# Kernel tuning notes

Measured on AMD Instinct MI355X. Metric: run time of the kernel, lower is better.

Reference implementation:

```python
import jax, jax.numpy as jnp
import numpy as np


def _chamfer_min_sqdist(a, b):
    # a: [N,3], b: [M,3] -> for each point in a, min squared distance to b. [N]
    # ||a||^2 + ||b||^2 - 2 a.b^T ; clamp tiny negatives from cancellation.
    a2 = jnp.sum(a * a, axis=-1)            # [N]
    b2 = jnp.sum(b * b, axis=-1)            # [M]
    cross = a @ b.T                          # [N,M] GEMM, K=3
    d = a2[:, None] + b2[None, :] - 2.0 * cross
    return jnp.maximum(jnp.min(d, axis=1), 0.0)


def setup_inputs() -> dict:
    key = jax.random.key(0)
    k1, k2 = jax.random.split(key)
    N = 16384
    state_x = jax.random.normal(k1, (N, 3), dtype=jnp.float32)
    target = jax.random.normal(k2, (N, 3), dtype=jnp.float32)
    return {"state_x": state_x, "target": target}


def reference(state_x, target):
    # dist1: target -> nearest in state_x ; dist2: state_x -> nearest in target
    dist1 = _chamfer_min_sqdist(target, state_x)   # [N]
    dist2 = _chamfer_min_sqdist(state_x, target)   # [N]
    loss = (jnp.mean(jnp.sqrt(dist1)) + jnp.mean(jnp.sqrt(dist2))) * 0.5
    return loss * 10.0
```

## Files before the change

kernel.cpp:

```cpp
#include <hip/hip_runtime.h>
#include <math.h>


typedef __attribute__((ext_vector_type(8)))  short bf16x8;
typedef __attribute__((ext_vector_type(16))) float f32x16;

#define S_SLICES 4

__device__ __forceinline__ unsigned enc_f32(float f) {
    int b = __float_as_int(f);
    return (b >= 0) ? ((unsigned)b | 0x80000000u) : ~(unsigned)b;
}
__device__ __forceinline__ float dec_f32(unsigned k) {
    int b = (k & 0x80000000u) ? (int)(k & 0x7FFFFFFFu) : ~(int)k;
    return __int_as_float(b);
}

__device__ __forceinline__ unsigned short f2bf(float v) {
    unsigned u = __float_as_uint(v);
    u += 0x7FFFu + ((u >> 16) & 1u);
    return (unsigned short)(u >> 16);
}
__device__ __forceinline__ float bf2f(unsigned short b) {
    unsigned u = ((unsigned)b) << 16;
    return __uint_as_float(u);
}
__device__ __forceinline__ unsigned pk2(unsigned short lo, unsigned short hi) {
    return (unsigned)lo | ((unsigned)hi << 16);
}

__device__ __forceinline__ f32x16 mfma_v(bf16x8 a, bf16x8 b, f32x16 c) {
    f32x16 d;
    asm("v_mfma_f32_32x32x16_bf16 %0, %1, %2, %3"
        : "=&v"(d) : "v"(a), "v"(b), "v"(c));
    return d;
}

__global__ __launch_bounds__(256) void chamfer_prep(
    const float* __restrict__ state_x, const float* __restrict__ target,
    uint4* __restrict__ AfragS, uint4* __restrict__ AfragT,
    uint4* __restrict__ BfragS, uint4* __restrict__ BfragT,
    unsigned* __restrict__ mins_u, float* __restrict__ out, int N)
{
    const int p = blockIdx.x * 256 + threadIdx.x;
    const float* src = (p < N) ? state_x : target;
    const int i = (p < N) ? p : p - N;

    const float x = src[3*i+0], y = src[3*i+1], z = src[3*i+2];
    const float n2 = fmaf(x, x, fmaf(y, y, z * z));

    const unsigned short hx = f2bf(x), hy = f2bf(y), hz = f2bf(z);
    const unsigned short lx = f2bf(x - bf2f(hx));
    const unsigned short ly = f2bf(y - bf2f(hy));
    const unsigned short lz = f2bf(z - bf2f(hz));
    const unsigned short mhx = f2bf(-2.0f*x), mhy = f2bf(-2.0f*y), mhz = f2bf(-2.0f*z);
    const unsigned short mlx = f2bf(-2.0f*x - bf2f(mhx));
    const unsigned short mly = f2bf(-2.0f*y - bf2f(mhy));
    const unsigned short mlz = f2bf(-2.0f*z - bf2f(mhz));
    const unsigned short hn = f2bf(n2);
    const unsigned short ln = f2bf(n2 - bf2f(hn));
    const unsigned short ONE = 0x3F80;

    uint4 A0 = make_uint4(pk2(mhx,mhy), pk2(mhz,mlx), pk2(mly,mlz), pk2(mhx,mhy));
    uint4 A1 = make_uint4(pk2(mhz,mlx), pk2(mly,mlz), pk2(hn,ln),   pk2(ONE,ONE));
    uint4 B0 = make_uint4(pk2(hx,hy), pk2(hz,hx), pk2(hy,hz), pk2(lx,ly));
    uint4 B1 = make_uint4(pk2(lz,lx), pk2(ly,lz), pk2(ONE,ONE), pk2(hn,ln));

    uint4* Aarr = (p < N) ? AfragS : AfragT;
    uint4* Barr = (p < N) ? BfragS : BfragT;
    Aarr[2*i+0] = A0;  Aarr[2*i+1] = A1;

    const int bbase = (i >> 6) * 128 + ((i >> 5) & 1) * 64 + (i & 31);
    Barr[bbase +  0] = B0;
    Barr[bbase + 32] = B1;

    mins_u[p] = 0xFFFFFFFFu;
    if (p == 0) *out = 0.0f;
}

__global__ __launch_bounds__(256, 4) void chamfer_main(
    const bf16x8* __restrict__ AfragS, const bf16x8* __restrict__ AfragT,
    const bf16x8* __restrict__ BfragS, const bf16x8* __restrict__ BfragT,
    unsigned* __restrict__ mins_u, int N, int S)
{
    const int tid  = threadIdx.x;
    const int lane = tid & 63;
    const int l31  = lane & 31;
    const int half = lane >> 5;
    const int w    = tid >> 6;

    const int bs = blockIdx.x / S;
    const int s  = blockIdx.x % S;
    const int qblk = bs * 128;

    const bf16x8* afr;
    const bf16x8* bfr;
    if (qblk < N) { afr = AfragT + (size_t)qblk * 2;       bfr = BfragS; }
    else          { afr = AfragS + (size_t)(qblk - N) * 2; bfr = BfragT; }

    const int CS = N / S;
    const int NCHUNK = CS / 1024;

    __shared__ uint4 ldsB[2048];
    const bf16x8* lb = (const bf16x8*)ldsB;

    const bf16x8 av = afr[(w * 32 + l31) * 2 + half];

    const int boff = half * 32 + l31;

    f32x16 racc, zc;
    #pragma unroll
    for (int i = 0; i < 16; ++i) { racc[i] = 3.0e38f; zc[i] = 0.0f; }

    for (int chunk = 0; chunk < NCHUNK; ++chunk) {
        {
            const uint4* src = (const uint4*)bfr
                             + ((size_t)s * CS + (size_t)chunk * 1024) * 2;
            #pragma unroll
            for (int j = 0; j < 8; ++j)
                ldsB[tid + j * 256] = src[tid + j * 256];
        }
        __syncthreads();

        #pragma unroll 1
        for (int it = 0; it < 16; ++it) {
            const bf16x8 b0 = lb[it * 128 + boff];
            const bf16x8 b1 = lb[it * 128 + 64 + boff];
            f32x16 a0 = mfma_v(av, b0, zc);
            f32x16 a1 = mfma_v(av, b1, zc);
            __builtin_amdgcn_sched_barrier(0);
            asm volatile("s_nop 7");
            asm volatile("s_nop 7");
            asm volatile("s_nop 7");
            __builtin_amdgcn_sched_barrier(0);
            #pragma unroll
            for (int i = 0; i < 16; ++i)
                racc[i] = fminf(fminf(racc[i], a0[i]), a1[i]);
        }
        __syncthreads();
    }

    float* lf = (float*)ldsB;
    const int cg = l31 >> 2, cl = l31 & 3;
    #pragma unroll
    for (int i = 0; i < 16; ++i) {
        const int row = (i & 3) + 8 * (i >> 2) + 4 * half;
        lf[w * 1024 + row * 32 + ((cg ^ (row & 7)) << 2) + cl] = racc[i];
    }
    __syncthreads();
    if (tid < 128) {
        const int r = tid & 31, wr = tid >> 5;
        const float4* rowp = (const float4*)(lf + wr * 1024 + r * 32);
        float m0 = 3.0e38f, m1 = 3.0e38f;
        #pragma unroll
        for (int g = 0; g < 8; g += 2) {
            const float4 v0 = rowp[g ^ (r & 7)];
            const float4 v1 = rowp[(g + 1) ^ (r & 7)];
            m0 = fminf(fminf(m0, v0.x), fminf(v0.y, v0.z));
            m0 = fminf(m0, v0.w);
            m1 = fminf(fminf(m1, v1.x), fminf(v1.y, v1.z));
            m1 = fminf(m1, v1.w);
        }
        atomicMin(&mins_u[qblk + wr * 32 + r], enc_f32(fminf(m0, m1)));
    }
}

__global__ __launch_bounds__(256) void chamfer_finish(
    const unsigned* __restrict__ mins_u, float* __restrict__ out, int N)
{
    const int tid = threadIdx.x;
    const int qi = blockIdx.x * 256 + tid;

    float v = sqrtf(fmaxf(dec_f32(mins_u[qi]), 0.0f));

    for (int off = 32; off > 0; off >>= 1) v += __shfl_down(v, off, 64);
    __shared__ float wsum[4];
    if ((tid & 63) == 0) wsum[tid >> 6] = v;
    __syncthreads();
    if (tid == 0) {
        const float bsum = wsum[0] + wsum[1] + wsum[2] + wsum[3];
        atomicAdd(out, bsum * 5.0f / (float)N);
    }
}

extern "C" void kernel_launch(void* const* d_in, const int* in_sizes, int n_in,
                              void* d_out, int out_size, void* d_ws, size_t ws_size,
                              hipStream_t stream)
{
    const float* state_x = (const float*)d_in[0];
    const float* target  = (const float*)d_in[1];
    float* out = (float*)d_out;

    const int N = in_sizes[0] / 3;
    const int twoN = 2 * N;

    int S = S_SLICES;
    while (S > 1 && (N % (S * 1024)) != 0) S >>= 1;

    char* wsb = (char*)d_ws;
    unsigned* mins_u = (unsigned*)wsb;
    uint4* AfragS = (uint4*)(wsb + (size_t)twoN * 4);
    uint4* AfragT = (uint4*)(wsb + (size_t)twoN * 4 + (size_t)N * 32);
    uint4* BfragS = (uint4*)(wsb + (size_t)twoN * 4 + (size_t)N * 64);
    uint4* BfragT = (uint4*)(wsb + (size_t)twoN * 4 + (size_t)N * 96);

    chamfer_prep<<<twoN / 256, 256, 0, stream>>>(
        state_x, target, AfragS, AfragT, BfragS, BfragT, mins_u, out, N);

    const int rowBlocks = twoN / 128;
    chamfer_main<<<rowBlocks * S, 256, 0, stream>>>(
        (const bf16x8*)AfragS, (const bf16x8*)AfragT,
        (const bf16x8*)BfragS, (const bf16x8*)BfragT, mins_u, N, S);

    chamfer_finish<<<twoN / 256, 256, 0, stream>>>(mins_u, out, N);
}
```

Measured before the change: 81.63 us.

## Compute one distance matrix and derive both directional minima from it

Exploits the symmetry of the pairwise distance matrix: only target-vs-state tiles are computed, and column minima are reduced via cross-half shuffles, LDS atomics and global atomics alongside the existing row minima. This removes half of the MFMA and fragment-preparation work and the second fragment set. It adds per-iteration reduction, shuffle and atomic overhead inside the hot loop, and doubles the slice count to keep the grid size up.

```diff
diff --git a/kernel.cpp b/kernel.cpp
--- a/kernel.cpp
+++ b/kernel.cpp
@@ -5,7 +5,7 @@
 typedef __attribute__((ext_vector_type(8)))  short bf16x8;
 typedef __attribute__((ext_vector_type(16))) float f32x16;
 
-#define S_SLICES 4
+#define S_SLICES 8
 
 __device__ __forceinline__ unsigned enc_f32(float f) {
     int b = __float_as_int(f);
@@ -38,49 +38,49 @@
 
 __global__ __launch_bounds__(256) void chamfer_prep(
     const float* __restrict__ state_x, const float* __restrict__ target,
-    uint4* __restrict__ AfragS, uint4* __restrict__ AfragT,
-    uint4* __restrict__ BfragS, uint4* __restrict__ BfragT,
+    uint4* __restrict__ AfragT, uint4* __restrict__ BfragS,
     unsigned* __restrict__ mins_u, float* __restrict__ out, int N)
 {
-    const int p = blockIdx.x * 256 + threadIdx.x;
-    const float* src = (p < N) ? state_x : target;
-    const int i = (p < N) ? p : p - N;
-
-    const float x = src[3*i+0], y = src[3*i+1], z = src[3*i+2];
-    const float n2 = fmaf(x, x, fmaf(y, y, z * z));
-
-    const unsigned short hx = f2bf(x), hy = f2bf(y), hz = f2bf(z);
-    const unsigned short lx = f2bf(x - bf2f(hx));
-    const unsigned short ly = f2bf(y - bf2f(hy));
-    const unsigned short lz = f2bf(z - bf2f(hz));
-    const unsigned short mhx = f2bf(-2.0f*x), mhy = f2bf(-2.0f*y), mhz = f2bf(-2.0f*z);
-    const unsigned short mlx = f2bf(-2.0f*x - bf2f(mhx));
-    const unsigned short mly = f2bf(-2.0f*y - bf2f(mhy));
-    const unsigned short mlz = f2bf(-2.0f*z - bf2f(mhz));
-    const unsigned short hn = f2bf(n2);
-    const unsigned short ln = f2bf(n2 - bf2f(hn));
-    const unsigned short ONE = 0x3F80;
-
-    uint4 A0 = make_uint4(pk2(mhx,mhy), pk2(mhz,mlx), pk2(mly,mlz), pk2(mhx,mhy));
-    uint4 A1 = make_uint4(pk2(mhz,mlx), pk2(mly,mlz), pk2(hn,ln),   pk2(ONE,ONE));
-    uint4 B0 = make_uint4(pk2(hx,hy), pk2(hz,hx), pk2(hy,hz), pk2(lx,ly));
-    uint4 B1 = make_uint4(pk2(lz,lx), pk2(ly,lz), pk2(ONE,ONE), pk2(hn,ln));
-
-    uint4* Aarr = (p < N) ? AfragS : AfragT;
-    uint4* Barr = (p < N) ? BfragS : BfragT;
-    Aarr[2*i+0] = A0;  Aarr[2*i+1] = A1;
-
-    const int bbase = (i >> 6) * 128 + ((i >> 5) & 1) * 64 + (i & 31);
-    Barr[bbase +  0] = B0;
-    Barr[bbase + 32] = B1;
-
-    mins_u[p] = 0xFFFFFFFFu;
-    if (p == 0) *out = 0.0f;
+    const int i = blockIdx.x * 256 + threadIdx.x;
+
+    {
+        const float x = target[3*i+0], y = target[3*i+1], z = target[3*i+2];
+        const float n2 = fmaf(x, x, fmaf(y, y, z * z));
+        const unsigned short mhx = f2bf(-2.0f*x), mhy = f2bf(-2.0f*y), mhz = f2bf(-2.0f*z);
+        const unsigned short mlx = f2bf(-2.0f*x - bf2f(mhx));
+        const unsigned short mly = f2bf(-2.0f*y - bf2f(mhy));
+        const unsigned short mlz = f2bf(-2.0f*z - bf2f(mhz));
+        const unsigned short hn = f2bf(n2);
+        const unsigned short ln = f2bf(n2 - bf2f(hn));
+        const unsigned short ONE = 0x3F80;
+        AfragT[2*i+0] = make_uint4(pk2(mhx,mhy), pk2(mhz,mlx), pk2(mly,mlz), pk2(mhx,mhy));
+        AfragT[2*i+1] = make_uint4(pk2(mhz,mlx), pk2(mly,mlz), pk2(hn,ln),   pk2(ONE,ONE));
+    }
+
+    {
+        const float x = state_x[3*i+0], y = state_x[3*i+1], z = state_x[3*i+2];
+        const float n2 = fmaf(x, x, fmaf(y, y, z * z));
+        const unsigned short hx = f2bf(x), hy = f2bf(y), hz = f2bf(z);
+        const unsigned short lx = f2bf(x - bf2f(hx));
+        const unsigned short ly = f2bf(y - bf2f(hy));
+        const unsigned short lz = f2bf(z - bf2f(hz));
+        const unsigned short hn = f2bf(n2);
+        const unsigned short ln = f2bf(n2 - bf2f(hn));
+        const unsigned short ONE = 0x3F80;
+        uint4 B0 = make_uint4(pk2(hx,hy), pk2(hz,hx), pk2(hy,hz), pk2(lx,ly));
+        uint4 B1 = make_uint4(pk2(lz,lx), pk2(ly,lz), pk2(ONE,ONE), pk2(hn,ln));
+        const int bbase = (i >> 6) * 128 + ((i >> 5) & 1) * 64 + (i & 31);
+        BfragS[bbase +  0] = B0;
+        BfragS[bbase + 32] = B1;
+    }
+
+    mins_u[i]     = 0xFFFFFFFFu;
+    mins_u[N + i] = 0xFFFFFFFFu;
+    if (i == 0) *out = 0.0f;
 }
 
 __global__ __launch_bounds__(256, 4) void chamfer_main(
-    const bf16x8* __restrict__ AfragS, const bf16x8* __restrict__ AfragT,
-    const bf16x8* __restrict__ BfragS, const bf16x8* __restrict__ BfragT,
+    const bf16x8* __restrict__ AfragT, const bf16x8* __restrict__ BfragS,
     unsigned* __restrict__ mins_u, int N, int S)
 {
     const int tid  = threadIdx.x;
@@ -93,15 +93,14 @@
     const int s  = blockIdx.x % S;
     const int qblk = bs * 128;
 
-    const bf16x8* afr;
-    const bf16x8* bfr;
-    if (qblk < N) { afr = AfragT + (size_t)qblk * 2;       bfr = BfragS; }
-    else          { afr = AfragS + (size_t)(qblk - N) * 2; bfr = BfragT; }
+    const bf16x8* afr = AfragT + (size_t)qblk * 2;
+    const bf16x8* bfr = BfragS;
 
     const int CS = N / S;
     const int NCHUNK = CS / 1024;
 
     __shared__ uint4 ldsB[2048];
+    __shared__ unsigned colmin[1024];
     const bf16x8* lb = (const bf16x8*)ldsB;
 
     const bf16x8 av = afr[(w * 32 + l31) * 2 + half];
@@ -120,6 +119,9 @@
             for (int j = 0; j < 8; ++j)
                 ldsB[tid + j * 256] = src[tid + j * 256];
         }
+        #pragma unroll
+        for (int j = 0; j < 4; ++j)
+            colmin[j * 256 + tid] = 0xFFFFFFFFu;
         __syncthreads();
 
         #pragma unroll 1
@@ -136,6 +138,26 @@
             #pragma unroll
             for (int i = 0; i < 16; ++i)
                 racc[i] = fminf(fminf(racc[i], a0[i]), a1[i]);
+            float c0 = fminf(a0[0], a0[1]);
+            float c1 = fminf(a1[0], a1[1]);
+            #pragma unroll
+            for (int i = 2; i < 16; i += 2) {
+                c0 = fminf(fminf(c0, a0[i]), a0[i + 1]);
+                c1 = fminf(fminf(c1, a1[i]), a1[i + 1]);
+            }
+            c0 = fminf(c0, __shfl_xor(c0, 32, 64));
+            c1 = fminf(c1, __shfl_xor(c1, 32, 64));
+            if (lane < 32) {
+                atomicMin(&colmin[it * 64 + lane],      enc_f32(c0));
+                atomicMin(&colmin[it * 64 + 32 + lane], enc_f32(c1));
+            }
+        }
+        __syncthreads();
+        {
+            const int colbase = N + s * CS + chunk * 1024;
+            #pragma unroll
+            for (int j = 0; j < 4; ++j)
+                atomicMin(&mins_u[colbase + j * 256 + tid], colmin[j * 256 + tid]);
         }
         __syncthreads();
     }
@@ -199,18 +221,15 @@
 
     char* wsb = (char*)d_ws;
     unsigned* mins_u = (unsigned*)wsb;
-    uint4* AfragS = (uint4*)(wsb + (size_t)twoN * 4);
-    uint4* AfragT = (uint4*)(wsb + (size_t)twoN * 4 + (size_t)N * 32);
-    uint4* BfragS = (uint4*)(wsb + (size_t)twoN * 4 + (size_t)N * 64);
-    uint4* BfragT = (uint4*)(wsb + (size_t)twoN * 4 + (size_t)N * 96);
-
-    chamfer_prep<<<twoN / 256, 256, 0, stream>>>(
-        state_x, target, AfragS, AfragT, BfragS, BfragT, mins_u, out, N);
-
-    const int rowBlocks = twoN / 128;
+    uint4* AfragT = (uint4*)(wsb + (size_t)twoN * 4);
+    uint4* BfragS = (uint4*)(wsb + (size_t)twoN * 4 + (size_t)N * 32);
+
+    chamfer_prep<<<N / 256, 256, 0, stream>>>(
+        state_x, target, AfragT, BfragS, mins_u, out, N);
+
+    const int rowBlocks = N / 128;
     chamfer_main<<<rowBlocks * S, 256, 0, stream>>>(
-        (const bf16x8*)AfragS, (const bf16x8*)AfragT,
-        (const bf16x8*)BfragS, (const bf16x8*)BfragT, mins_u, N, S);
+        (const bf16x8*)AfragT, (const bf16x8*)BfragS, mins_u, N, S);
 
     chamfer_finish<<<twoN / 256, 256, 0, stream>>>(mins_u, out, N);
 }
```

After: 81.16 us. No clear change (-0.6%).
